# Kernel tuning notes

Measured on AMD Instinct MI355X. Metric: run time of the kernel, lower is better.

## Reference

```python
import jax, jax.numpy as jnp
import numpy as np

EPS = 1e-6
MAX_ITER = 50
LAMBDAS = (0.5, 0.5)


def matrix_sqrt_inv_sqrt(Sigma):
    # truncated SVD with singular values clamped at EPS (matches torch code)
    U, S, Vh = jnp.linalg.svd(Sigma, full_matrices=False)
    S = jnp.clip(S, EPS, None)
    s_sqrt = jnp.sqrt(S)
    Sigma_sqrt = (U * s_sqrt) @ Vh          # U diag(sqrt(S)) V^T
    Sigma_inv_sqrt = (U * (1.0 / s_sqrt)) @ Vh
    return Sigma_sqrt, Sigma_inv_sqrt


def gaussian_stats(x):
    # x: [n, d]
    mean = jnp.mean(x, axis=0)
    xc = x - mean
    cov = (xc.T @ xc) / (x.shape[0] - 1)
    return mean, cov


def barycenter_cov(cov_list, lambdas, cov_init):
    def body(Sigma_old, _):
        S_sqrt, S_inv_sqrt = matrix_sqrt_inv_sqrt(Sigma_old)
        Sigma_new = jnp.zeros_like(Sigma_old)
        for lam, cov_j in zip(lambdas, cov_list):
            middle = S_sqrt @ cov_j @ S_sqrt
            middle_sqrt, _ = matrix_sqrt_inv_sqrt(middle)
            Sigma_new = Sigma_new + lam * (S_inv_sqrt @ middle_sqrt @ S_inv_sqrt)
        Sigma_old = 0.5 * (Sigma_new + Sigma_new.T)  # symmetrize
        return Sigma_old, None

    Sigma, _ = jax.lax.scan(body, cov_init, None, length=MAX_ITER)
    return Sigma


def apply_barycenter_transform(x, mu_c, cov_c, mu_b, cov_b):
    Sc_sqrt, Sc_inv_sqrt = matrix_sqrt_inv_sqrt(cov_c)
    middle = Sc_sqrt @ cov_b @ Sc_sqrt
    middle_sqrt, _ = matrix_sqrt_inv_sqrt(middle)
    M = Sc_inv_sqrt @ middle_sqrt @ Sc_inv_sqrt
    return (x - mu_c) @ M.T + mu_b


def setup_inputs() -> dict:
    key = jax.random.key(0)
    k1, k2 = jax.random.split(key)
    content = jax.random.normal(k1, (1, 512, 256, 256), dtype=jnp.float32)
    style = jax.random.normal(k2, (1, 512, 256, 256), dtype=jnp.float32)
    return {"content": content, "style": style, "level": 3}


def reference(content, style, level):
    d, n1, n2 = content.shape[1], content.shape[2], content.shape[3]
    x = content.reshape(-1, d)      # faithful to torch reshape(-1, d)
    s = style.reshape(-1, d)
    mean_c, cov_c = gaussian_stats(x)
    mean_s, cov_s = gaussian_stats(s)
    # j0 = argmax(lambdas) = 0 -> init with content covariance
    mean_bary = LAMBDAS[0] * mean_c + LAMBDAS[1] * mean_s
    cov_bary = barycenter_cov((cov_c, cov_s), LAMBDAS, cov_c)
    out = apply_barycenter_transform(x, mean_c, cov_c, mean_bary, cov_bary)
    return out.reshape(1, d, n1, n2)
```

## Files before the change

### kernel.cpp

```cpp
#include <hip/hip_runtime.h>

#define NROWS 65536
#define DD 512
#define MSZ (DD * DD)
#define NS_ITERS 7
#define BARY_ITERS 16
#define KSPLIT 8
#define KCHUNK (NROWS / KSPLIT)

__global__ __launch_bounds__(512) void colsum_kernel(const float* __restrict__ X,
                                                     const float* __restrict__ S,
                                                     float* __restrict__ sums) {
    const float* src = (blockIdx.y == 0) ? X : S;
    float* dst = sums + blockIdx.y * DD;
    int col = threadIdx.x;
    long base = (long)blockIdx.x * 256 * DD;
    float acc = 0.f;
    #pragma unroll 8
    for (int r = 0; r < 256; ++r)
        acc += src[base + (long)r * DD + col];
    atomicAdd(dst + col, acc);
}

__global__ __launch_bounds__(512) void finalize_mean_kernel(float* __restrict__ ws) {
    int t = threadIdx.x;
    const float inv_n = 1.f / (float)NROWS;
    float mc = ws[t] * inv_n;
    float ms = ws[DD + t] * inv_n;
    ws[t] = mc;
    ws[DD + t] = ms;
    ws[2 * DD + t] = 0.5f * (mc + ms);
}

__global__ __launch_bounds__(256) void covsyrk_kernel(const float* __restrict__ X,
                                                      const float* __restrict__ S,
                                                      float* __restrict__ G) {
    if (blockIdx.x > blockIdx.y) return;
    __shared__ float As[16][68];
    __shared__ float Bs[16][68];
    int mat = blockIdx.z / KSPLIT;
    int ks  = blockIdx.z % KSPLIT;
    const float* src = (mat == 0) ? X : S;
    float* g = G + (long)mat * MSZ;
    int a0 = blockIdx.x * 64, b0 = blockIdx.y * 64;
    int t = threadIdx.x;
    int rr = t >> 4;
    int c4 = (t & 15) << 2;
    int tx = t & 15, ty = t >> 4;
    float acc[4][4] = {};
    long r0 = (long)ks * KCHUNK;
    for (int k0 = 0; k0 < KCHUNK; k0 += 16) {
        long base = (r0 + k0 + rr) * DD;
        float4 av = *(const float4*)(src + base + a0 + c4);
        float4 bv = *(const float4*)(src + base + b0 + c4);
        *(float4*)&As[rr][c4] = av;
        *(float4*)&Bs[rr][c4] = bv;
        __syncthreads();
        #pragma unroll
        for (int kk = 0; kk < 16; ++kk) {
            float4 a = *(const float4*)&As[kk][ty << 2];
            float4 b = *(const float4*)&Bs[kk][tx << 2];
            float af[4] = {a.x, a.y, a.z, a.w};
            float bf[4] = {b.x, b.y, b.z, b.w};
            #pragma unroll
            for (int i = 0; i < 4; ++i)
                #pragma unroll
                for (int j = 0; j < 4; ++j)
                    acc[i][j] += af[i] * bf[j];
        }
        __syncthreads();
    }
    #pragma unroll
    for (int i = 0; i < 4; ++i)
        #pragma unroll
        for (int j = 0; j < 4; ++j)
            atomicAdd(&g[(long)(a0 + ty * 4 + i) * DD + b0 + tx * 4 + j], acc[i][j]);
}

__global__ __launch_bounds__(512) void covfix_kernel(const float* __restrict__ Gt,
                                                     float* __restrict__ C,
                                                     const float* __restrict__ means) {
    int m = blockIdx.y, i = blockIdx.x, j = threadIdx.x;
    const float* mu = means + m * DD;
    const float* g = Gt + (long)m * MSZ;
    int ii = i, jj = j;
    if ((ii >> 6) > (jj >> 6)) { int tmp = ii; ii = jj; jj = tmp; }
    float v = g[(long)ii * DD + jj];
    C[(long)m * MSZ + (long)i * DD + j] =
        (v - (float)NROWS * mu[i] * mu[j]) * (1.f / (float)(NROWS - 1));
}

__global__ __launch_bounds__(512) void trace_kernel(const float* __restrict__ Abase, long long stride,
                                                    float* __restrict__ slotbase, long long slotstride) {
    __shared__ float red[512];
    const float* A = Abase + (long long)blockIdx.x * stride;
    int t = threadIdx.x;
    red[t] = A[(long)t * DD + t];
    __syncthreads();
    for (int s = 256; s > 0; s >>= 1) {
        if (t < s) red[t] += red[t + s];
        __syncthreads();
    }
    if (t == 0) {
        float c = 2.5f * red[0] / (float)DD;
        float* sl = slotbase + (long long)blockIdx.x * slotstride;
        sl[0] = c;
        sl[1] = 1.f / c;
        sl[2] = sqrtf(c);
        sl[3] = 1.f / sqrtf(c);
    }
}

__global__ __launch_bounds__(512) void nsinit_kernel(const float* __restrict__ Abase, long long sA,
                                                     float* __restrict__ Ybase, long long sY,
                                                     float* __restrict__ Zbase, long long sZ,
                                                     const float* __restrict__ slotbase, long long slotstride) {
    int z = blockIdx.y;
    const float* A = Abase + (long long)z * sA;
    float* Y = Ybase + (long long)z * sY;
    float* Z = Zbase + (long long)z * sZ;
    float invc = slotbase[(long long)z * slotstride + 1];
    int idx = blockIdx.x * 512 + threadIdx.x;
    int row = idx >> 9, col = idx & 511;
    Y[idx] = A[idx] * invc;
    Z[idx] = (row == col) ? 1.f : 0.f;
}

__global__ __launch_bounds__(256) void mm512_kernel(const float* __restrict__ Ab, long long sA,
                                                    const float* __restrict__ Bb, long long sB,
                                                    const float* __restrict__ Db, long long sD,
                                                    float* __restrict__ Cb, long long sC,
                                                    float alpha, float beta,
                                                    const float* __restrict__ alphaPtr) {
    __shared__ float As[32][36];
    __shared__ float Bs[32][36];
    long long z = blockIdx.z;
    const float* A = Ab + z * sA;
    const float* B = Bb + z * sB;
    const float* Dm = Db + z * sD;
    float* C = Cb + z * sC;
    int i0 = blockIdx.y * 32, j0 = blockIdx.x * 32;
    int t = threadIdx.x;
    int lr = t >> 3;
    int lc4 = (t & 7) << 2;
    int tx = t & 15, ty = t >> 4;
    float acc[2][2] = {};
    for (int k0 = 0; k0 < DD; k0 += 32) {
        float4 av = *(const float4*)(A + (long)(i0 + lr) * DD + k0 + lc4);
        float4 bv = *(const float4*)(B + (long)(k0 + lr) * DD + j0 + lc4);
        As[lc4 + 0][lr] = av.x; As[lc4 + 1][lr] = av.y;
        As[lc4 + 2][lr] = av.z; As[lc4 + 3][lr] = av.w;
        *(float4*)&Bs[lr][lc4] = bv;
        __syncthreads();
        #pragma unroll
        for (int kk = 0; kk < 32; ++kk) {
            float2 a = *(const float2*)&As[kk][ty << 1];
            float2 b = *(const float2*)&Bs[kk][tx << 1];
            acc[0][0] += a.x * b.x; acc[0][1] += a.x * b.y;
            acc[1][0] += a.y * b.x; acc[1][1] += a.y * b.y;
        }
        __syncthreads();
    }
    float aeff = alpha * (alphaPtr ? *alphaPtr : 1.f);
    #pragma unroll
    for (int i = 0; i < 2; ++i)
        #pragma unroll
        for (int j = 0; j < 2; ++j) {
            long idx = (long)(i0 + (ty << 1) + i) * DD + j0 + (tx << 1) + j;
            float v = aeff * acc[i][j];
            if (beta != 0.f) v += beta * Dm[idx];
            C[idx] = v;
        }
}

__global__ __launch_bounds__(512) void combineQ_kernel(const float* __restrict__ Y0,
                                                       const float* __restrict__ Y1,
                                                       const float* __restrict__ sl1,
                                                       const float* __restrict__ sl2,
                                                       float* __restrict__ Q) {
    int idx = blockIdx.x * 512 + threadIdx.x;
    Q[idx] = 0.5f * (sl1[2] * Y0[idx] + sl2[2] * Y1[idx]);
}

__global__ __launch_bounds__(512) void symmetrize_kernel(const float* __restrict__ V,
                                                         float* __restrict__ Sg) {
    int i = blockIdx.x, j = threadIdx.x;
    Sg[(long)i * DD + j] = 0.5f * (V[(long)i * DD + j] + V[(long)j * DD + i]);
}

__global__ __launch_bounds__(64) void bias_kernel(const float* __restrict__ M,
                                                  const float* __restrict__ means,
                                                  float* __restrict__ bias) {
    int j = blockIdx.x;
    int lane = threadIdx.x;
    const float* mu_c = means;
    const float* mu_b = means + 2 * DD;
    float p = 0.f;
    for (int k = lane; k < DD; k += 64)
        p += mu_c[k] * M[(long)j * DD + k];
    #pragma unroll
    for (int off = 32; off > 0; off >>= 1)
        p += __shfl_down(p, off, 64);
    if (lane == 0) bias[j] = mu_b[j] - p;
}

__global__ __launch_bounds__(256) void outgemm_kernel(const float* __restrict__ X,
                                                      const float* __restrict__ M,
                                                      const float* __restrict__ bias,
                                                      float* __restrict__ out) {
    __shared__ float As[16][68];
    __shared__ float Bs[16][68];
    int j0 = blockIdx.x * 64;
    int i0 = blockIdx.y * 64;
    int t = threadIdx.x;
    int lr = t >> 2;
    int lc4 = (t & 3) << 2;
    int tx = t & 15, ty = t >> 4;
    float acc[4][4] = {};
    for (int k0 = 0; k0 < DD; k0 += 16) {
        float4 xa = *(const float4*)(X + (long)(i0 + lr) * DD + k0 + lc4);
        float4 mb = *(const float4*)(M + (long)(j0 + lr) * DD + k0 + lc4);
        As[lc4 + 0][lr] = xa.x; As[lc4 + 1][lr] = xa.y;
        As[lc4 + 2][lr] = xa.z; As[lc4 + 3][lr] = xa.w;
        Bs[lc4 + 0][lr] = mb.x; Bs[lc4 + 1][lr] = mb.y;
        Bs[lc4 + 2][lr] = mb.z; Bs[lc4 + 3][lr] = mb.w;
        __syncthreads();
        #pragma unroll
        for (int kk = 0; kk < 16; ++kk) {
            float4 a = *(const float4*)&As[kk][ty << 2];
            float4 b = *(const float4*)&Bs[kk][tx << 2];
            float af[4] = {a.x, a.y, a.z, a.w};
            float bf[4] = {b.x, b.y, b.z, b.w};
            #pragma unroll
            for (int i = 0; i < 4; ++i)
                #pragma unroll
                for (int j = 0; j < 4; ++j)
                    acc[i][j] += af[i] * bf[j];
        }
        __syncthreads();
    }
    #pragma unroll
    for (int i = 0; i < 4; ++i)
        #pragma unroll
        for (int j = 0; j < 4; ++j)
            out[(long)(i0 + ty * 4 + i) * DD + j0 + tx * 4 + j] =
                acc[i][j] + bias[j0 + tx * 4 + j];
}

extern "C" void kernel_launch(void* const* d_in, const int* in_sizes, int n_in,
                              void* d_out, int out_size, void* d_ws, size_t ws_size,
                              hipStream_t stream) {
    const float* X = (const float*)d_in[0];
    const float* S = (const float*)d_in[1];
    float* out = (float*)d_out;
    float* ws = (float*)d_ws;

    float* bias  = ws + 1536;
    float* slot0 = ws + 2048;
    float* slot1 = ws + 2056;
    float* MATS  = ws + 4096;
    auto m = [&](int i) { return MATS + (long long)i * MSZ; };
    float* covc  = m(0);
    float* Sigma = m(2);
    float* Gtmp  = m(22);

    hipMemsetAsync(ws, 0, 1024 * sizeof(float), stream);
    hipMemsetAsync(Gtmp, 0, 2ll * MSZ * sizeof(float), stream);

    colsum_kernel<<<dim3(256, 2), 512, 0, stream>>>(X, S, ws);
    finalize_mean_kernel<<<1, 512, 0, stream>>>(ws);
    covsyrk_kernel<<<dim3(8, 8, 2 * KSPLIT), 256, 0, stream>>>(X, S, Gtmp);
    covfix_kernel<<<dim3(512, 2), 512, 0, stream>>>(Gtmp, covc, ws);
    hipMemcpyAsync(Sigma, covc, MSZ * sizeof(float), hipMemcpyDeviceToDevice, stream);

    auto mm = [&](const float* A, long long sA, const float* B, long long sB,
                  const float* Dm, long long sD, float* C, long long sC,
                  float alpha, float beta, const float* aptr, int batch) {
        mm512_kernel<<<dim3(16, 16, batch), 256, 0, stream>>>(A, sA, B, sB, Dm, sD, C, sC,
                                                              alpha, beta, aptr);
    };

    auto ns_single = [&](const float* Ain, float* slots, float*& Yout, float*& Zout) {
        trace_kernel<<<1, 512, 0, stream>>>(Ain, 0, slots, 0);
        nsinit_kernel<<<dim3(512, 1), 512, 0, stream>>>(Ain, 0, m(3), 0, m(4), 0, slots, 0);
        float *Y = m(3), *Z = m(4), *Yn = m(5), *Zn = m(6), *W = m(7);
        for (int it = 0; it < NS_ITERS; ++it) {
            mm(Z, 0, Y, 0, W, 0, W, 0, 1.f, 0.f, nullptr, 1);
            mm(Y, W - Y, W, Z - W, Y, Z - Y, Yn, Zn - Yn, -0.5f, 1.5f, nullptr, 2);
            float* tp = Y; Y = Yn; Yn = tp;
            tp = Z; Z = Zn; Zn = tp;
        }
        Yout = Y; Zout = Z;
    };

    auto ns_batch = [&](const float* Abase, int nb, float* slots, float*& Yout) {
        trace_kernel<<<nb, 512, 0, stream>>>(Abase, MSZ, slots, 8);
        nsinit_kernel<<<dim3(512, nb), 512, 0, stream>>>(Abase, MSZ, m(10), MSZ, m(14), MSZ, slots, 8);
        float *Y = m(10), *Z = m(14), *Yn = m(16), *Zn = m(18), *W = m(12);
        for (int it = 0; it < NS_ITERS; ++it) {
            mm(Z, MSZ, Y, MSZ, W, MSZ, W, MSZ, 1.f, 0.f, nullptr, nb);
            mm(Y, MSZ, W, MSZ, Y, MSZ, Yn, MSZ, -0.5f, 1.5f, nullptr, nb);
            mm(W, MSZ, Z, MSZ, Z, MSZ, Zn, MSZ, -0.5f, 1.5f, nullptr, nb);
            float* tp = Y; Y = Yn; Yn = tp;
            tp = Z; Z = Zn; Zn = tp;
        }
        Yout = Y;
    };

    float *Ysig, *Zsig, *Ybc;
    for (int iter = 0; iter < BARY_ITERS; ++iter) {
        ns_single(Sigma, slot0, Ysig, Zsig);
        mm(Ysig, 0, covc, MSZ, m(8), MSZ, m(8), MSZ, 1.f, 0.f, nullptr, 2);
        mm(m(8), MSZ, Ysig, 0, m(20), MSZ, m(20), MSZ, 1.f, 0.f, slot0, 2);
        ns_batch(m(20), 2, slot1, Ybc);
        combineQ_kernel<<<512, 512, 0, stream>>>(Ybc, Ybc + MSZ, slot1, slot1 + 8, m(9));
        mm(Zsig, 0, m(9), 0, m(7), 0, m(7), 0, 1.f, 0.f, nullptr, 1);
        mm(m(7), 0, Zsig, 0, m(8), 0, m(8), 0, 1.f, 0.f, slot0 + 1, 1);
        symmetrize_kernel<<<512, 512, 0, stream>>>(m(8), Sigma);
    }

    ns_single(covc, slot0, Ysig, Zsig);
    mm(Ysig, 0, Sigma, 0, m(8), 0, m(8), 0, 1.f, 0.f, nullptr, 1);
    mm(m(8), 0, Ysig, 0, m(20), 0, m(20), 0, 1.f, 0.f, slot0, 1);
    ns_batch(m(20), 1, slot1, Ybc);
    mm(Zsig, 0, Ybc, 0, m(7), 0, m(7), 0, 1.f, 0.f, slot1 + 2, 1);
    mm(m(7), 0, Zsig, 0, m(8), 0, m(8), 0, 1.f, 0.f, slot0 + 1, 1);
    bias_kernel<<<512, 64, 0, stream>>>(m(8), ws, bias);
    outgemm_kernel<<<dim3(8, 1024), 256, 0, stream>>>(X, m(8), bias, out);
}
```

Baseline: 15.79 ms.

## Use 128x128 register-tiled split-K GEMMs with separate reduction for 512 matmuls

```diff
diff --git a/kernel.cpp b/kernel.cpp
--- a/kernel.cpp
+++ b/kernel.cpp
@@ -5,8 +5,8 @@
 #define MSZ (DD * DD)
 #define NS_ITERS 7
 #define BARY_ITERS 16
-#define KSPLIT 8
-#define KCHUNK (NROWS / KSPLIT)
+#define CSPLIT 16
+#define CCHUNK (NROWS / CSPLIT)
 
 __global__ __launch_bounds__(512) void colsum_kernel(const float* __restrict__ X,
                                                      const float* __restrict__ S,
@@ -32,49 +32,67 @@
     ws[2 * DD + t] = 0.5f * (mc + ms);
 }
 
-__global__ __launch_bounds__(256) void covsyrk_kernel(const float* __restrict__ X,
-                                                      const float* __restrict__ S,
-                                                      float* __restrict__ G) {
-    if (blockIdx.x > blockIdx.y) return;
-    __shared__ float As[16][68];
-    __shared__ float Bs[16][68];
-    int mat = blockIdx.z / KSPLIT;
-    int ks  = blockIdx.z % KSPLIT;
-    const float* src = (mat == 0) ? X : S;
-    float* g = G + (long)mat * MSZ;
-    int a0 = blockIdx.x * 64, b0 = blockIdx.y * 64;
+__global__ __launch_bounds__(256) void covsyrk2_kernel(const float* __restrict__ X,
+                                                       const float* __restrict__ S,
+                                                       float* __restrict__ G) {
+    int ta = blockIdx.x >> 2, tb = blockIdx.x & 3;
+    if (ta > tb) return;
+    int a0 = ta << 7, b0 = tb << 7;
+    const float* src = (blockIdx.z == 0) ? X : S;
+    float* g = G + (long long)blockIdx.z * MSZ;
+    long kbase = (long)blockIdx.y * CCHUNK;
+    __shared__ float As[32][140];
+    __shared__ float Bs[32][140];
     int t = threadIdx.x;
-    int rr = t >> 4;
-    int c4 = (t & 15) << 2;
-    int tx = t & 15, ty = t >> 4;
-    float acc[4][4] = {};
-    long r0 = (long)ks * KCHUNK;
-    for (int k0 = 0; k0 < KCHUNK; k0 += 16) {
-        long base = (r0 + k0 + rr) * DD;
-        float4 av = *(const float4*)(src + base + a0 + c4);
-        float4 bv = *(const float4*)(src + base + b0 + c4);
-        *(float4*)&As[rr][c4] = av;
-        *(float4*)&Bs[rr][c4] = bv;
+    int kr = t >> 5;
+    int c4 = (t & 31) << 2;
+    int sc = c4 + ((c4 >> 5) << 2);
+    int iy = t >> 4, ix = t & 15;
+    int aoff = (iy << 3) + ((iy >> 2) << 2);
+    int boff = (ix << 3) + ((ix >> 2) << 2);
+    float acc[8][8] = {};
+    float4 pa[4], pb[4];
+    #pragma unroll
+    for (int p = 0; p < 4; ++p) {
+        long row = (kbase + kr + p * 8) * DD;
+        pa[p] = *(const float4*)(src + row + a0 + c4);
+        pb[p] = *(const float4*)(src + row + b0 + c4);
+    }
+    for (int kb = 0; kb < CCHUNK; kb += 32) {
         __syncthreads();
         #pragma unroll
-        for (int kk = 0; kk < 16; ++kk) {
-            float4 a = *(const float4*)&As[kk][ty << 2];
-            float4 b = *(const float4*)&Bs[kk][tx << 2];
-            float af[4] = {a.x, a.y, a.z, a.w};
-            float bf[4] = {b.x, b.y, b.z, b.w};
-            #pragma unroll
-            for (int i = 0; i < 4; ++i)
+        for (int p = 0; p < 4; ++p) {
+            *(float4*)&As[kr + p * 8][sc] = pa[p];
+            *(float4*)&Bs[kr + p * 8][sc] = pb[p];
+        }
+        __syncthreads();
+        if (kb + 32 < CCHUNK) {
+            #pragma unroll
+            for (int p = 0; p < 4; ++p) {
+                long row = (kbase + kb + 32 + kr + p * 8) * DD;
+                pa[p] = *(const float4*)(src + row + a0 + c4);
+                pb[p] = *(const float4*)(src + row + b0 + c4);
+            }
+        }
+        #pragma unroll 4
+        for (int kk = 0; kk < 32; ++kk) {
+            float a[8], bf[8];
+            *(float4*)&a[0] = *(const float4*)&As[kk][aoff];
+            *(float4*)&a[4] = *(const float4*)&As[kk][aoff + 4];
+            *(float4*)&bf[0] = *(const float4*)&Bs[kk][boff];
+            *(float4*)&bf[4] = *(const float4*)&Bs[kk][boff + 4];
+            #pragma unroll
+            for (int i = 0; i < 8; ++i)
                 #pragma unroll
-                for (int j = 0; j < 4; ++j)
-                    acc[i][j] += af[i] * bf[j];
-        }
-        __syncthreads();
-    }
-    #pragma unroll
-    for (int i = 0; i < 4; ++i)
+                for (int j = 0; j < 8; ++j)
+                    acc[i][j] += a[i] * bf[j];
+        }
+    }
+    #pragma unroll
+    for (int i = 0; i < 8; ++i)
         #pragma unroll
-        for (int j = 0; j < 4; ++j)
-            atomicAdd(&g[(long)(a0 + ty * 4 + i) * DD + b0 + tx * 4 + j], acc[i][j]);
+        for (int j = 0; j < 8; ++j)
+            atomicAdd(&g[(long)(a0 + (iy << 3) + i) * DD + b0 + (ix << 3) + j], acc[i][j]);
 }
 
 __global__ __launch_bounds__(512) void covfix_kernel(const float* __restrict__ Gt,
@@ -84,7 +102,7 @@
     const float* mu = means + m * DD;
     const float* g = Gt + (long)m * MSZ;
     int ii = i, jj = j;
-    if ((ii >> 6) > (jj >> 6)) { int tmp = ii; ii = jj; jj = tmp; }
+    if ((ii >> 7) > (jj >> 7)) { int tmp = ii; ii = jj; jj = tmp; }
     float v = g[(long)ii * DD + jj];
     C[(long)m * MSZ + (long)i * DD + j] =
         (v - (float)NROWS * mu[i] * mu[j]) * (1.f / (float)(NROWS - 1));
@@ -126,51 +144,99 @@
     Z[idx] = (row == col) ? 1.f : 0.f;
 }
 
-__global__ __launch_bounds__(256) void mm512_kernel(const float* __restrict__ Ab, long long sA,
-                                                    const float* __restrict__ Bb, long long sB,
-                                                    const float* __restrict__ Db, long long sD,
-                                                    float* __restrict__ Cb, long long sC,
-                                                    float alpha, float beta,
-                                                    const float* __restrict__ alphaPtr) {
-    __shared__ float As[32][36];
-    __shared__ float Bs[32][36];
-    long long z = blockIdx.z;
-    const float* A = Ab + z * sA;
-    const float* B = Bb + z * sB;
-    const float* Dm = Db + z * sD;
-    float* C = Cb + z * sC;
-    int i0 = blockIdx.y * 32, j0 = blockIdx.x * 32;
+__global__ __launch_bounds__(256) void mmk(const float* __restrict__ A, long long sA,
+                                           const float* __restrict__ B, long long sB,
+                                           float* __restrict__ pool) {
+    int ks = gridDim.y;
+    int b = blockIdx.z, s = blockIdx.y;
+    int i0 = (blockIdx.x >> 2) << 7;
+    int j0 = (blockIdx.x & 3) << 7;
+    int Ks = DD / ks;
+    int kbase = s * Ks;
+    const float* Ab = A + (long long)b * sA;
+    const float* Bb = B + (long long)b * sB;
+    __shared__ float As[32][132];
+    __shared__ float Bs[32][140];
     int t = threadIdx.x;
-    int lr = t >> 3;
-    int lc4 = (t & 7) << 2;
-    int tx = t & 15, ty = t >> 4;
-    float acc[2][2] = {};
-    for (int k0 = 0; k0 < DD; k0 += 32) {
-        float4 av = *(const float4*)(A + (long)(i0 + lr) * DD + k0 + lc4);
-        float4 bv = *(const float4*)(B + (long)(k0 + lr) * DD + j0 + lc4);
-        As[lc4 + 0][lr] = av.x; As[lc4 + 1][lr] = av.y;
-        As[lc4 + 2][lr] = av.z; As[lc4 + 3][lr] = av.w;
-        *(float4*)&Bs[lr][lc4] = bv;
+    int iy = t >> 4, ix = t & 15;
+    int ldr = t >> 3;
+    int ldc = (t & 7) << 2;
+    int boff = (ix << 3) + ((ix >> 2) << 2);
+    float acc[8][8] = {};
+    float4 pa[4], pb[4];
+    #pragma unroll
+    for (int p = 0; p < 4; ++p) {
+        pa[p] = *(const float4*)(Ab + (long)(i0 + ldr + p * 32) * DD + kbase + ldc);
+        pb[p] = *(const float4*)(Bb + (long)(kbase + ldr) * DD + j0 + ldc + p * 32);
+    }
+    for (int kb = 0; kb < Ks; kb += 32) {
         __syncthreads();
         #pragma unroll
+        for (int p = 0; p < 4; ++p) {
+            int r = ldr + p * 32;
+            As[ldc + 0][r] = pa[p].x; As[ldc + 1][r] = pa[p].y;
+            As[ldc + 2][r] = pa[p].z; As[ldc + 3][r] = pa[p].w;
+            int q = (ldc + p * 32) >> 2;
+            *(float4*)&Bs[ldr][(q << 2) + ((q >> 3) << 2)] = pb[p];
+        }
+        __syncthreads();
+        if (kb + 32 < Ks) {
+            int k0 = kbase + kb + 32;
+            #pragma unroll
+            for (int p = 0; p < 4; ++p) {
+                pa[p] = *(const float4*)(Ab + (long)(i0 + ldr + p * 32) * DD + k0 + ldc);
+                pb[p] = *(const float4*)(Bb + (long)(k0 + ldr) * DD + j0 + ldc + p * 32);
+            }
+        }
+        #pragma unroll 4
         for (int kk = 0; kk < 32; ++kk) {
-            float2 a = *(const float2*)&As[kk][ty << 1];
-            float2 b = *(const float2*)&Bs[kk][tx << 1];
-            acc[0][0] += a.x * b.x; acc[0][1] += a.x * b.y;
-            acc[1][0] += a.y * b.x; acc[1][1] += a.y * b.y;
-        }
-        __syncthreads();
-    }
-    float aeff = alpha * (alphaPtr ? *alphaPtr : 1.f);
-    #pragma unroll
-    for (int i = 0; i < 2; ++i)
-        #pragma unroll
-        for (int j = 0; j < 2; ++j) {
-            long idx = (long)(i0 + (ty << 1) + i) * DD + j0 + (tx << 1) + j;
-            float v = aeff * acc[i][j];
-            if (beta != 0.f) v += beta * Dm[idx];
-            C[idx] = v;
-        }
+            float a[8], bf[8];
+            *(float4*)&a[0] = *(const float4*)&As[kk][iy << 3];
+            *(float4*)&a[4] = *(const float4*)&As[kk][(iy << 3) + 4];
+            *(float4*)&bf[0] = *(const float4*)&Bs[kk][boff];
+            *(float4*)&bf[4] = *(const float4*)&Bs[kk][boff + 4];
+            #pragma unroll
+            for (int i = 0; i < 8; ++i)
+                #pragma unroll
+                for (int j = 0; j < 8; ++j)
+                    acc[i][j] += a[i] * bf[j];
+        }
+    }
+    float* P = pool + (long long)(b * ks + s) * MSZ;
+    #pragma unroll
+    for (int i = 0; i < 8; ++i) {
+        long off = (long)(i0 + (iy << 3) + i) * DD + j0 + (ix << 3);
+        *(float4*)(P + off) = *(float4*)&acc[i][0];
+        *(float4*)(P + off + 4) = *(float4*)&acc[i][4];
+    }
+}
+
+__global__ __launch_bounds__(256) void reduce_kernel(const float* __restrict__ pool, int ks,
+        const float* __restrict__ D1, long long sD1,
+        const float* __restrict__ D2, long long sD2, int dsplit,
+        float* __restrict__ C1, long long sC1,
+        float* __restrict__ C2, long long sC2, int csplit,
+        float alpha, float beta, const float* __restrict__ aptr) {
+    int b = blockIdx.y;
+    long idx = (long)blockIdx.x * 1024 + (threadIdx.x << 2);
+    const float* P = pool + (long long)b * ks * MSZ + idx;
+    float4 acc = *(const float4*)P;
+    for (int k = 1; k < ks; ++k) {
+        float4 v = *(const float4*)(P + (long long)k * MSZ);
+        acc.x += v.x; acc.y += v.y; acc.z += v.z; acc.w += v.w;
+    }
+    float aeff = alpha * (aptr ? *aptr : 1.f);
+    acc.x *= aeff; acc.y *= aeff; acc.z *= aeff; acc.w *= aeff;
+    if (beta != 0.f) {
+        const float* D = (b < dsplit) ? D1 + (long long)b * sD1
+                                      : D2 + (long long)(b - dsplit) * sD2;
+        float4 d = *(const float4*)(D + idx);
+        acc.x += beta * d.x; acc.y += beta * d.y;
+        acc.z += beta * d.z; acc.w += beta * d.w;
+    }
+    float* C = (b < csplit) ? C1 + (long long)b * sC1
+                            : C2 + (long long)(b - csplit) * sC2;
+    *(float4*)(C + idx) = acc;
 }
 
 __global__ __launch_bounds__(512) void combineQ_kernel(const float* __restrict__ Y0,
@@ -204,47 +270,72 @@
     if (lane == 0) bias[j] = mu_b[j] - p;
 }
 
-__global__ __launch_bounds__(256) void outgemm_kernel(const float* __restrict__ X,
-                                                      const float* __restrict__ M,
-                                                      const float* __restrict__ bias,
-                                                      float* __restrict__ out) {
-    __shared__ float As[16][68];
-    __shared__ float Bs[16][68];
-    int j0 = blockIdx.x * 64;
-    int i0 = blockIdx.y * 64;
+__global__ __launch_bounds__(256) void outgemm2_kernel(const float* __restrict__ X,
+                                                       const float* __restrict__ M,
+                                                       const float* __restrict__ bias,
+                                                       float* __restrict__ out) {
+    int j0 = blockIdx.x << 7;
+    int i0 = blockIdx.y << 7;
+    __shared__ float As[32][132];
+    __shared__ float Bs[32][140];
     int t = threadIdx.x;
-    int lr = t >> 2;
-    int lc4 = (t & 3) << 2;
-    int tx = t & 15, ty = t >> 4;
-    float acc[4][4] = {};
-    for (int k0 = 0; k0 < DD; k0 += 16) {
-        float4 xa = *(const float4*)(X + (long)(i0 + lr) * DD + k0 + lc4);
-        float4 mb = *(const float4*)(M + (long)(j0 + lr) * DD + k0 + lc4);
-        As[lc4 + 0][lr] = xa.x; As[lc4 + 1][lr] = xa.y;
-        As[lc4 + 2][lr] = xa.z; As[lc4 + 3][lr] = xa.w;
-        Bs[lc4 + 0][lr] = mb.x; Bs[lc4 + 1][lr] = mb.y;
-        Bs[lc4 + 2][lr] = mb.z; Bs[lc4 + 3][lr] = mb.w;
+    int iy = t >> 4, ix = t & 15;
+    int ldr = t >> 3;
+    int ldc = (t & 7) << 2;
+    int boff = (ix << 3) + ((ix >> 2) << 2);
+    float acc[8][8] = {};
+    float4 pa[4], pb[4];
+    #pragma unroll
+    for (int p = 0; p < 4; ++p) {
+        pa[p] = *(const float4*)(X + (long)(i0 + ldr + p * 32) * DD + ldc);
+        pb[p] = *(const float4*)(M + (long)(j0 + ldr + p * 32) * DD + ldc);
+    }
+    for (int kb = 0; kb < DD; kb += 32) {
         __syncthreads();
         #pragma unroll
-        for (int kk = 0; kk < 16; ++kk) {
-            float4 a = *(const float4*)&As[kk][ty << 2];
-            float4 b = *(const float4*)&Bs[kk][tx << 2];
-            float af[4] = {a.x, a.y, a.z, a.w};
-            float bf[4] = {b.x, b.y, b.z, b.w};
-            #pragma unroll
-            for (int i = 0; i < 4; ++i)
+        for (int p = 0; p < 4; ++p) {
+            int r = ldr + p * 32;
+            As[ldc + 0][r] = pa[p].x; As[ldc + 1][r] = pa[p].y;
+            As[ldc + 2][r] = pa[p].z; As[ldc + 3][r] = pa[p].w;
+            int q = r >> 2;
+            int bc = (q << 2) + ((q >> 3) << 2) + (r & 3);
+            Bs[ldc + 0][bc] = pb[p].x; Bs[ldc + 1][bc] = pb[p].y;
+            Bs[ldc + 2][bc] = pb[p].z; Bs[ldc + 3][bc] = pb[p].w;
+        }
+        __syncthreads();
+        if (kb + 32 < DD) {
+            #pragma unroll
+            for (int p = 0; p < 4; ++p) {
+                pa[p] = *(const float4*)(X + (long)(i0 + ldr + p * 32) * DD + kb + 32 + ldc);
+                pb[p] = *(const float4*)(M + (long)(j0 + ldr + p * 32) * DD + kb + 32 + ldc);
+            }
+        }
+        #pragma unroll 4
+        for (int kk = 0; kk < 32; ++kk) {
+            float a[8], bf[8];
+            *(float4*)&a[0] = *(const float4*)&As[kk][iy << 3];
+            *(float4*)&a[4] = *(const float4*)&As[kk][(iy << 3) + 4];
+            *(float4*)&bf[0] = *(const float4*)&Bs[kk][boff];
+            *(float4*)&bf[4] = *(const float4*)&Bs[kk][boff + 4];
+            #pragma unroll
+            for (int i = 0; i < 8; ++i)
                 #pragma unroll
-                for (int j = 0; j < 4; ++j)
-                    acc[i][j] += af[i] * bf[j];
-        }
-        __syncthreads();
-    }
-    #pragma unroll
-    for (int i = 0; i < 4; ++i)
-        #pragma unroll
-        for (int j = 0; j < 4; ++j)
-            out[(long)(i0 + ty * 4 + i) * DD + j0 + tx * 4 + j] =
-                acc[i][j] + bias[j0 + tx * 4 + j];
+                for (int j = 0; j < 8; ++j)
+                    acc[i][j] += a[i] * bf[j];
+        }
+    }
+    float4 bv0 = *(const float4*)(bias + j0 + (ix << 3));
+    float4 bv1 = *(const float4*)(bias + j0 + (ix << 3) + 4);
+    #pragma unroll
+    for (int i = 0; i < 8; ++i) {
+        long off = (long)(i0 + (iy << 3) + i) * DD + j0 + (ix << 3);
+        float4 v0 = *(float4*)&acc[i][0];
+        float4 v1 = *(float4*)&acc[i][4];
+        v0.x += bv0.x; v0.y += bv0.y; v0.z += bv0.z; v0.w += bv0.w;
+        v1.x += bv1.x; v1.y += bv1.y; v1.z += bv1.z; v1.w += bv1.w;
+        *(float4*)(out + off) = v0;
+        *(float4*)(out + off + 4) = v1;
+    }
 }
 
 extern "C" void kernel_launch(void* const* d_in, const int* in_sizes, int n_in,
@@ -254,77 +345,79 @@
     const float* S = (const float*)d_in[1];
     float* out = (float*)d_out;
     float* ws = (float*)d_ws;
+    float* pool = out;
 
     float* bias  = ws + 1536;
     float* slot0 = ws + 2048;
     float* slot1 = ws + 2056;
     float* MATS  = ws + 4096;
-    auto m = [&](int i) { return MATS + (long long)i * MSZ; };
-    float* covc  = m(0);
-    float* Sigma = m(2);
-    float* Gtmp  = m(22);
+    auto m_ = [&](int i) { return MATS + (long long)i * MSZ; };
+    float* covc  = m_(0);
+    float* Sigma = m_(2);
+    float* Q     = m_(6);
+    float* mid   = m_(7);
 
     hipMemsetAsync(ws, 0, 1024 * sizeof(float), stream);
-    hipMemsetAsync(Gtmp, 0, 2ll * MSZ * sizeof(float), stream);
+    hipMemsetAsync(pool, 0, 2ll * MSZ * sizeof(float), stream);
 
     colsum_kernel<<<dim3(256, 2), 512, 0, stream>>>(X, S, ws);
     finalize_mean_kernel<<<1, 512, 0, stream>>>(ws);
-    covsyrk_kernel<<<dim3(8, 8, 2 * KSPLIT), 256, 0, stream>>>(X, S, Gtmp);
-    covfix_kernel<<<dim3(512, 2), 512, 0, stream>>>(Gtmp, covc, ws);
+    covsyrk2_kernel<<<dim3(16, CSPLIT, 2), 256, 0, stream>>>(X, S, pool);
+    covfix_kernel<<<dim3(512, 2), 512, 0, stream>>>(pool, covc, ws);
     hipMemcpyAsync(Sigma, covc, MSZ * sizeof(float), hipMemcpyDeviceToDevice, stream);
 
     auto mm = [&](const float* A, long long sA, const float* B, long long sB,
-                  const float* Dm, long long sD, float* C, long long sC,
+                  const float* D1, long long sD1, const float* D2, long long sD2, int dsplit,
+                  float* C1, long long sC1, float* C2, long long sC2, int csplit,
                   float alpha, float beta, const float* aptr, int batch) {
-        mm512_kernel<<<dim3(16, 16, batch), 256, 0, stream>>>(A, sA, B, sB, Dm, sD, C, sC,
-                                                              alpha, beta, aptr);
+        int ks = 16 / batch;
+        mmk<<<dim3(16, ks, batch), 256, 0, stream>>>(A, sA, B, sB, pool);
+        reduce_kernel<<<dim3(256, batch), 256, 0, stream>>>(pool, ks, D1, sD1, D2, sD2, dsplit,
+                                                            C1, sC1, C2, sC2, csplit,
+                                                            alpha, beta, aptr);
     };
-
-    auto ns_single = [&](const float* Ain, float* slots, float*& Yout, float*& Zout) {
-        trace_kernel<<<1, 512, 0, stream>>>(Ain, 0, slots, 0);
-        nsinit_kernel<<<dim3(512, 1), 512, 0, stream>>>(Ain, 0, m(3), 0, m(4), 0, slots, 0);
-        float *Y = m(3), *Z = m(4), *Yn = m(5), *Zn = m(6), *W = m(7);
+    auto mms = [&](const float* A, long long sA, const float* B, long long sB,
+                   float* C, long long sC, float alpha, const float* aptr, int batch) {
+        mm(A, sA, B, sB, nullptr, 0, nullptr, 0, batch,
+           C, sC, nullptr, 0, batch, alpha, 0.f, aptr, batch);
+    };
+
+    auto ns = [&](float* base, const float* Ain, long long sAin, int nb, float* slots) {
+        float* Y = base;
+        float* W = base + (long long)nb * MSZ;
+        float* Z = base + 2ll * nb * MSZ;
+        trace_kernel<<<nb, 512, 0, stream>>>(Ain, sAin, slots, 8);
+        nsinit_kernel<<<dim3(512, nb), 512, 0, stream>>>(Ain, sAin, Y, MSZ, Z, MSZ, slots, 8);
         for (int it = 0; it < NS_ITERS; ++it) {
-            mm(Z, 0, Y, 0, W, 0, W, 0, 1.f, 0.f, nullptr, 1);
-            mm(Y, W - Y, W, Z - W, Y, Z - Y, Yn, Zn - Yn, -0.5f, 1.5f, nullptr, 2);
-            float* tp = Y; Y = Yn; Yn = tp;
-            tp = Z; Z = Zn; Zn = tp;
-        }
-        Yout = Y; Zout = Z;
+            mms(Z, MSZ, Y, MSZ, W, MSZ, 1.f, nullptr, nb);
+            mm(Y, MSZ, W, MSZ,
+               Y, MSZ, Z, MSZ, nb,
+               Y, MSZ, Z, MSZ, nb,
+               -0.5f, 1.5f, nullptr, 2 * nb);
+        }
     };
 
-    auto ns_batch = [&](const float* Abase, int nb, float* slots, float*& Yout) {
-        trace_kernel<<<nb, 512, 0, stream>>>(Abase, MSZ, slots, 8);
-        nsinit_kernel<<<dim3(512, nb), 512, 0, stream>>>(Abase, MSZ, m(10), MSZ, m(14), MSZ, slots, 8);
-        float *Y = m(10), *Z = m(14), *Yn = m(16), *Zn = m(18), *W = m(12);
-        for (int it = 0; it < NS_ITERS; ++it) {
-            mm(Z, MSZ, Y, MSZ, W, MSZ, W, MSZ, 1.f, 0.f, nullptr, nb);
-            mm(Y, MSZ, W, MSZ, Y, MSZ, Yn, MSZ, -0.5f, 1.5f, nullptr, nb);
-            mm(W, MSZ, Z, MSZ, Z, MSZ, Zn, MSZ, -0.5f, 1.5f, nullptr, nb);
-            float* tp = Y; Y = Yn; Yn = tp;
-            tp = Z; Z = Zn; Zn = tp;
-        }
-        Yout = Y;
-    };
-
-    float *Ysig, *Zsig, *Ybc;
+    float* Ysig = m_(3);
+    float* Zsig = m_(5);
+    float* Yb   = m_(9);
+
     for (int iter = 0; iter < BARY_ITERS; ++iter) {
-        ns_single(Sigma, slot0, Ysig, Zsig);
-        mm(Ysig, 0, covc, MSZ, m(8), MSZ, m(8), MSZ, 1.f, 0.f, nullptr, 2);
-        mm(m(8), MSZ, Ysig, 0, m(20), MSZ, m(20), MSZ, 1.f, 0.f, slot0, 2);
-        ns_batch(m(20), 2, slot1, Ybc);
-        combineQ_kernel<<<512, 512, 0, stream>>>(Ybc, Ybc + MSZ, slot1, slot1 + 8, m(9));
-        mm(Zsig, 0, m(9), 0, m(7), 0, m(7), 0, 1.f, 0.f, nullptr, 1);
-        mm(m(7), 0, Zsig, 0, m(8), 0, m(8), 0, 1.f, 0.f, slot0 + 1, 1);
-        symmetrize_kernel<<<512, 512, 0, stream>>>(m(8), Sigma);
-    }
-
-    ns_single(covc, slot0, Ysig, Zsig);
-    mm(Ysig, 0, Sigma, 0, m(8), 0, m(8), 0, 1.f, 0.f, nullptr, 1);
-    mm(m(8), 0, Ysig, 0, m(20), 0, m(20), 0, 1.f, 0.f, slot0, 1);
-    ns_batch(m(20), 1, slot1, Ybc);
-    mm(Zsig, 0, Ybc, 0, m(7), 0, m(7), 0, 1.f, 0.f, slot1 + 2, 1);
-    mm(m(7), 0, Zsig, 0, m(8), 0, m(8), 0, 1.f, 0.f, slot0 + 1, 1);
-    bias_kernel<<<512, 64, 0, stream>>>(m(8), ws, bias);
-    outgemm_kernel<<<dim3(8, 1024), 256, 0, stream>>>(X, m(8), bias, out);
-}
+        ns(m_(3), Sigma, 0, 1, slot0);
+        mms(Ysig, 0, covc, MSZ, m_(9), MSZ, 1.f, nullptr, 2);
+        mms(m_(9), MSZ, Ysig, 0, mid, MSZ, 1.f, slot0, 2);
+        ns(m_(9), mid, MSZ, 2, slot1);
+        combineQ_kernel<<<512, 512, 0, stream>>>(m_(9), m_(10), slot1, slot1 + 8, Q);
+        mms(Zsig, 0, Q, 0, m_(4), 0, 1.f, nullptr, 1);
+        mms(m_(4), 0, Zsig, 0, mid, 0, 1.f, slot0 + 1, 1);
+        symmetrize_kernel<<<512, 512, 0, stream>>>(mid, Sigma);
+    }
+
+    ns(m_(3), covc, 0, 1, slot0);
+    mms(Ysig, 0, Sigma, 0, m_(9), 0, 1.f, nullptr, 1);
+    mms(m_(9), 0, Ysig, 0, mid, 0, 1.f, slot0, 1);
+    ns(m_(9), mid, 0, 1, slot1);
+    mms(Zsig, 0, Yb, 0, m_(4), 0, 1.f, slot1 + 2, 1);
+    mms(m_(4), 0, Zsig, 0, Q, 0, 1.f, slot0 + 1, 1);
+    bias_kernel<<<512, 64, 0, stream>>>(Q, ws, bias);
+    outgemm2_kernel<<<dim3(4, 512), 256, 0, stream>>>(X, Q, bias, out);
+}
```

New measurement: 16.14 ms. 2.2% more time.
